# Optimization experiments

Hardware: AMD Instinct MI355X
Metric: run time of the kernel (lower is better)

Reference implementation:

```python
import jax, jax.numpy as jnp
import numpy as np

R, B, D, H, N, F = 8, 16, 32, 128, 2048, 256
HALF_LOG_2PI = np.float32(0.9189385332046727)  # 0.5*log(2*pi)


def _made_masks():
    # MADE masks for a 2-hidden-layer network (D -> H -> H -> 2*D), params=2,
    # input_order='random' per (region, batch) network, hidden degrees cyclic in [1, D-1].
    rng = np.random.RandomState(0)
    deg_in = np.stack([np.stack([rng.permutation(D) + 1 for _ in range(B)]) for _ in range(R)])  # [R,B,D]
    h_deg = (np.arange(H) % (D - 1)) + 1  # [H]
    M1 = (deg_in[:, :, :, None] <= h_deg[None, None, None, :]).astype(np.float32)  # [R,B,D,H]
    M2 = np.broadcast_to((h_deg[:, None] <= h_deg[None, :]).astype(np.float32), (R, B, H, H)).copy()  # [R,B,H,H]
    out_deg = np.repeat(deg_in, 2, axis=-1)  # [R,B,2D]; index k=2*d+p matches reshape(...,D,2)
    M3 = (h_deg[None, None, :, None] < out_deg[:, :, None, :]).astype(np.float32)  # [R,B,H,2D]
    return M1, M2, M3


def setup_inputs() -> dict:
    key = jax.random.key(0)
    k1, k2, k3, k4 = jax.random.split(key, 4)
    x = jax.random.normal(k1, (N, F), dtype=jnp.float32)
    W1 = jax.random.normal(k2, (R, B, D, H), dtype=jnp.float32) * 0.1
    W2 = jax.random.normal(k3, (R, B, H, H), dtype=jnp.float32) * 0.05
    W3 = jax.random.normal(k4, (R, B, H, 2 * D), dtype=jnp.float32) * 0.02
    M1, M2, M3 = _made_masks()
    region_idx = jnp.arange(F, dtype=jnp.int64 if jax.config.jax_enable_x64 else jnp.int32).reshape(R, D)
    return {"x": x, "W1": W1, "W2": W2, "W3": W3,
            "M1": jnp.asarray(M1), "M2": jnp.asarray(M2), "M3": jnp.asarray(M3),
            "region_idx": region_idx}


def reference(x, W1, W2, W3, M1, M2, M3, region_idx):
    # Gather per-region features: [N, R, D] -> [R, N, D]
    xr = jnp.transpose(x[:, region_idx], (1, 0, 2))
    # Masked MADE forward (no bias, relu), batched over all R*B networks.
    h1 = jax.nn.relu(jnp.einsum('rnd,rbdh->rbnh', xr, W1 * M1))
    h2 = jax.nn.relu(jnp.einsum('rbnh,rbhk->rbnk', h1, W2 * M2))
    out = jnp.einsum('rbnk,rbko->rbno', h2, W3 * M3)  # [R,B,N,2D]
    out = out.reshape(out.shape[0], out.shape[1], out.shape[2], -1, 2)  # [R,B,N,D,2]
    shift, log_scale = out[..., 0], out[..., 1]
    # MAF inverse (one pass): u = (y - shift) * exp(-log_scale);
    # log_prob = sum_d Normal(0,1).log_prob(u_d) - log_scale_d
    u = (xr[:, None] - shift) * jnp.exp(-log_scale)  # [R,B,N,D]
    ll = jnp.sum(-0.5 * u * u - HALF_LOG_2PI - log_scale, axis=-1)  # [R,B,N]
    return jnp.transpose(ll, (2, 0, 1))  # [N, R, B]
```

## Files before the change

kernel.cpp:

```cpp
#include <hip/hip_runtime.h>
#include <math.h>

constexpr int R_ = 8;
constexpr int B_ = 16;
constexpr int D_ = 32;
constexpr int H_ = 128;
constexpr int N_ = 2048;
constexpr int F_ = 256;
constexpr int O_ = 64;
constexpr float HLP_ = 0.9189385332046727f;

typedef float f32x4 __attribute__((ext_vector_type(4)));
typedef short bf16x8 __attribute__((ext_vector_type(8)));
typedef unsigned uint32x4 __attribute__((ext_vector_type(4)));

__device__ __forceinline__ unsigned pk2(float lo, float hi) {
    unsigned a = __builtin_bit_cast(unsigned, lo) + 0x8000u;
    unsigned b = __builtin_bit_cast(unsigned, hi) + 0x8000u;
    return __builtin_amdgcn_perm(b, a, 0x07060302);
}

__global__ __launch_bounds__(512, 2)
void flow_all(const float* __restrict__ x,
              const float* __restrict__ W1, const float* __restrict__ W2,
              const float* __restrict__ W3,
              const float* __restrict__ M1, const float* __restrict__ M2,
              const float* __restrict__ M3,
              const int* __restrict__ ridx,
              float* __restrict__ out)
{
    __shared__ __align__(16) unsigned short WA1[8  * 64 * 8];
    __shared__ __align__(16) unsigned short WA2[32 * 64 * 8];
    __shared__ __align__(16) unsigned short WA3[16 * 64 * 8];
    __shared__ __align__(16) unsigned short hws[8 * 4096];

    const int bid  = blockIdx.x;
    const int rb   = bid >> 1;
    const int half = bid & 1;
    const int r    = rb >> 4;

    const int t    = threadIdx.x;
    const int lane = t & 63;
    const int w    = t >> 6;
    const int q    = lane >> 4;
    const int c    = lane & 15;

    unsigned short* hwp = hws + w * 4096;

    const int nbase = half * 1024 + w * 16 + c;

    int cols[8];
#pragma unroll
    for (int j = 0; j < 8; ++j) cols[j] = ridx[r * 32 + q * 8 + j];

    float gA[8], gB[8];
    {
        const float* ra = x + (size_t)nbase * F_;
        const float* rb2 = ra + (size_t)128 * F_;
#pragma unroll
        for (int j = 0; j < 8; ++j) { gA[j] = ra[cols[j]]; gB[j] = rb2[cols[j]]; }
    }

    {
        const float* W1b = W1 + (size_t)rb * 32 * 128;
        const float* M1b = M1 + (size_t)rb * 32 * 128;
        const float* W2b = W2 + (size_t)rb * 128 * 128;
        const float* M2s = M2;
        const float* W3b = W3 + (size_t)rb * 128 * 64;
        const float* M3b = M3 + (size_t)rb * 128 * 64;

        const int pm = t & 127, pkq = t >> 7;
        const int qm = t & 63,  qkq = t >> 6;
        int osrc;
        {
            int dp = qm >> 1, pb = qm & 1;
            int dsrc = ((dp >> 1) & 3) * 8 + (dp >> 3) * 2 + (dp & 1);
            osrc = dsrc * 2 + pb;
        }

        float wv[2][8], mv[2][8];
        auto slab_load = [&](int s, float* wvv, float* mvv) {
            if (s == 0) {
                const float* wp = W1b + (size_t)(pkq * 8) * 128 + pm;
                const float* mp = M1b + (size_t)(pkq * 8) * 128 + pm;
#pragma unroll
                for (int e = 0; e < 8; ++e) { wvv[e] = wp[(size_t)e * 128]; mvv[e] = mp[(size_t)e * 128]; }
            } else if (s <= 4) {
                const float* wp = W2b + (size_t)((s - 1) * 32 + pkq * 8) * 128 + pm;
                const float* mp = M2s + (size_t)((s - 1) * 32 + pkq * 8) * 128 + pm;
#pragma unroll
                for (int e = 0; e < 8; ++e) { wvv[e] = wp[(size_t)e * 128]; mvv[e] = mp[(size_t)e * 128]; }
            } else {
                int ss = s - 5;
                const float* wp = W3b + (size_t)(ss * 64 + qkq * 8) * 64 + osrc;
                const float* mp = M3b + (size_t)(ss * 64 + qkq * 8) * 64 + osrc;
#pragma unroll
                for (int e = 0; e < 8; ++e) { wvv[e] = wp[(size_t)e * 64]; mvv[e] = mp[(size_t)e * 64]; }
            }
        };
        auto slab_store = [&](int s, const float* wvv, const float* mvv) {
            unsigned u0 = pk2(wvv[0] * mvv[0], wvv[1] * mvv[1]);
            unsigned u1 = pk2(wvv[2] * mvv[2], wvv[3] * mvv[3]);
            unsigned u2 = pk2(wvv[4] * mvv[4], wvv[5] * mvv[5]);
            unsigned u3 = pk2(wvv[6] * mvv[6], wvv[7] * mvv[7]);
            uint32x4 u = {u0, u1, u2, u3};
            if (s == 0) {
                int mt = pm >> 4, l = pkq * 16 + (pm & 15);
                *(uint32x4*)&WA1[(mt * 64 + l) * 8] = u;
            } else if (s <= 4) {
                int kt = s - 1, mt = pm >> 4, l = pkq * 16 + (pm & 15);
                *(uint32x4*)&WA2[((kt * 8 + mt) * 64 + l) * 8] = u;
            } else {
                int ss = s - 5;
                int kt = ss * 2 + (qkq >> 2), mt3 = qm >> 4, l = (qkq & 3) * 16 + (qm & 15);
                *(uint32x4*)&WA3[((kt * 4 + mt3) * 64 + l) * 8] = u;
            }
        };

        slab_load(0, wv[0], mv[0]);
#pragma unroll
        for (int s = 0; s < 7; ++s) {
            if (s < 6) slab_load(s + 1, wv[(s + 1) & 1], mv[(s + 1) & 1]);
            slab_store(s, wv[s & 1], mv[s & 1]);
        }
    }
    __syncthreads();

    const f32x4 z = {0.f, 0.f, 0.f, 0.f};
#pragma unroll 1
    for (int p = 0; p < 4; ++p) {
        float xA[8], xB[8];
#pragma unroll
        for (int j = 0; j < 8; ++j) { xA[j] = gA[j]; xB[j] = gB[j]; }
        uint32x4 uA = {pk2(xA[0], xA[1]), pk2(xA[2], xA[3]), pk2(xA[4], xA[5]), pk2(xA[6], xA[7])};
        uint32x4 uB = {pk2(xB[0], xB[1]), pk2(xB[2], xB[3]), pk2(xB[4], xB[5]), pk2(xB[6], xB[7])};
        bf16x8 xbA = __builtin_bit_cast(bf16x8, uA);
        bf16x8 xbB = __builtin_bit_cast(bf16x8, uB);

        auto hstore = [&](int tau, int mt, const f32x4& v) {
            int ktw = mt >> 1;
            int qw  = (mt & 1) * 2 + (q >> 1);
            int j0  = (q & 1) * 4;
            unsigned lo = pk2(fmaxf(v[0], 0.f), fmaxf(v[1], 0.f));
            unsigned hi = pk2(fmaxf(v[2], 0.f), fmaxf(v[3], 0.f));
            *(uint2*)&hwp[(((tau * 4 + ktw) * 64) + qw * 16 + c) * 8 + j0] = make_uint2(lo, hi);
        };

        {
            bf16x8 a_[8];
#pragma unroll
            for (int mt = 0; mt < 8; ++mt)
                a_[mt] = *(const bf16x8*)&WA1[(mt * 64 + lane) * 8];
            f32x4 accA[8], accB[8];
#pragma unroll
            for (int mt = 0; mt < 8; ++mt) {
                accA[mt] = __builtin_amdgcn_mfma_f32_16x16x32_bf16(a_[mt], xbA, z, 0, 0, 0);
                accB[mt] = __builtin_amdgcn_mfma_f32_16x16x32_bf16(a_[mt], xbB, z, 0, 0, 0);
            }
#pragma unroll
            for (int mt = 0; mt < 8; ++mt) { hstore(0, mt, accA[mt]); hstore(1, mt, accB[mt]); }
        }

        if (p < 3) {
            const float* ra = x + (size_t)(nbase + (p + 1) * 256) * F_;
            const float* rb2 = ra + (size_t)128 * F_;
#pragma unroll
            for (int j = 0; j < 8; ++j) { gA[j] = ra[cols[j]]; gB[j] = rb2[cols[j]]; }
        }

        {
            f32x4 acc2A[8], acc2B[8];
#pragma unroll
            for (int mt = 0; mt < 8; ++mt) { acc2A[mt] = z; acc2B[mt] = z; }
#pragma unroll
            for (int kt = 0; kt < 4; ++kt) {
                bf16x8 bA = *(const bf16x8*)&hwp[((0 + kt) * 64 + lane) * 8];
                bf16x8 bB = *(const bf16x8*)&hwp[((4 + kt) * 64 + lane) * 8];
                bf16x8 a2_[8];
#pragma unroll
                for (int mt = 0; mt < 8; ++mt)
                    a2_[mt] = *(const bf16x8*)&WA2[((kt * 8 + mt) * 64 + lane) * 8];
#pragma unroll
                for (int mt = 0; mt < 8; ++mt) {
                    acc2A[mt] = __builtin_amdgcn_mfma_f32_16x16x32_bf16(a2_[mt], bA, acc2A[mt], 0, 0, 0);
                    acc2B[mt] = __builtin_amdgcn_mfma_f32_16x16x32_bf16(a2_[mt], bB, acc2B[mt], 0, 0, 0);
                }
            }
#pragma unroll
            for (int mt = 0; mt < 8; ++mt) { hstore(0, mt, acc2A[mt]); hstore(1, mt, acc2B[mt]); }
        }

        {
            f32x4 acc3A[4], acc3B[4];
#pragma unroll
            for (int mt3 = 0; mt3 < 4; ++mt3) { acc3A[mt3] = z; acc3B[mt3] = z; }
#pragma unroll
            for (int kt = 0; kt < 4; ++kt) {
                bf16x8 bA = *(const bf16x8*)&hwp[((0 + kt) * 64 + lane) * 8];
                bf16x8 bB = *(const bf16x8*)&hwp[((4 + kt) * 64 + lane) * 8];
                bf16x8 a3_[4];
#pragma unroll
                for (int mt3 = 0; mt3 < 4; ++mt3)
                    a3_[mt3] = *(const bf16x8*)&WA3[((kt * 4 + mt3) * 64 + lane) * 8];
#pragma unroll
                for (int mt3 = 0; mt3 < 4; ++mt3) {
                    acc3A[mt3] = __builtin_amdgcn_mfma_f32_16x16x32_bf16(a3_[mt3], bA, acc3A[mt3], 0, 0, 0);
                    acc3B[mt3] = __builtin_amdgcn_mfma_f32_16x16x32_bf16(a3_[mt3], bB, acc3B[mt3], 0, 0, 0);
                }
            }
            float llA = 0.f, llB = 0.f;
#pragma unroll
            for (int mt3 = 0; mt3 < 4; ++mt3) {
#pragma unroll
                for (int rr = 0; rr < 2; ++rr) {
                    float shA = acc3A[mt3][rr * 2], lsA = acc3A[mt3][rr * 2 + 1];
                    float shB = acc3B[mt3][rr * 2], lsB = acc3B[mt3][rr * 2 + 1];
                    float u0 = (xA[mt3 * 2 + rr] - shA) * __expf(-lsA);
                    float u1 = (xB[mt3 * 2 + rr] - shB) * __expf(-lsB);
                    llA += fmaf(-0.5f * u0, u0, -HLP_ - lsA);
                    llB += fmaf(-0.5f * u1, u1, -HLP_ - lsB);
                }
            }
            llA += __shfl_xor(llA, 16, 64);  llA += __shfl_xor(llA, 32, 64);
            llB += __shfl_xor(llB, 16, 64);  llB += __shfl_xor(llB, 32, 64);
            if (q == 0) {
                int n = nbase + p * 256;
                out[(size_t)n * 128 + rb]         = llA;
                out[(size_t)(n + 128) * 128 + rb] = llB;
            }
        }
    }
}

extern "C" void kernel_launch(void* const* d_in, const int* in_sizes, int n_in,
                              void* d_out, int out_size, void* d_ws, size_t ws_size,
                              hipStream_t stream) {
    const float* x   = (const float*)d_in[0];
    const float* W1  = (const float*)d_in[1];
    const float* W2  = (const float*)d_in[2];
    const float* W3  = (const float*)d_in[3];
    const float* M1  = (const float*)d_in[4];
    const float* M2  = (const float*)d_in[5];
    const float* M3  = (const float*)d_in[6];
    const int*  ridx = (const int*)d_in[7];
    float* out = (float*)d_out;

    flow_all<<<dim3(256), dim3(512), 0, stream>>>(x, W1, W2, W3, M1, M2, M3, ridx, out);
}
```

Measured before the change: 109.7 us.

## Hold masked weight fragments in registers and halve block size to 4 waves

The masked bf16 weight fragments for all three layers now stay in VGPRs for the whole kernel. They are built through a small double-buffered LDS staging area with a barrier per slab, so the main loop no longer reads weights from LDS. Blocks shrink to 256 threads with launch bounds (256,1), and each wave handles a contiguous 256-row chunk over 8 iterations instead of 4. This removes repeated LDS weight reads per MFMA but uses many more registers (about 352 VGPRs of A fragments) and leaves fewer waves to hide latency.

```diff
diff --git a/kernel.cpp b/kernel.cpp
--- a/kernel.cpp
+++ b/kernel.cpp
@@ -20,7 +20,7 @@
     return __builtin_amdgcn_perm(b, a, 0x07060302);
 }
 
-__global__ __launch_bounds__(512, 2)
+__global__ __launch_bounds__(256, 1)
 void flow_all(const float* __restrict__ x,
               const float* __restrict__ W1, const float* __restrict__ W2,
               const float* __restrict__ W3,
@@ -29,15 +29,13 @@
               const int* __restrict__ ridx,
               float* __restrict__ out)
 {
-    __shared__ __align__(16) unsigned short WA1[8  * 64 * 8];
-    __shared__ __align__(16) unsigned short WA2[32 * 64 * 8];
-    __shared__ __align__(16) unsigned short WA3[16 * 64 * 8];
-    __shared__ __align__(16) unsigned short hws[8 * 4096];
-
-    const int bid  = blockIdx.x;
-    const int rb   = bid >> 1;
-    const int half = bid & 1;
-    const int r    = rb >> 4;
+    __shared__ __align__(16) unsigned short stg[2][5120];
+    __shared__ __align__(16) unsigned short hws[4][4096];
+
+    const int bid = blockIdx.x;
+    const int rb  = bid >> 1;
+    const int hf  = bid & 1;
+    const int r   = rb >> 4;
 
     const int t    = threadIdx.x;
     const int lane = t & 63;
@@ -45,9 +43,9 @@
     const int q    = lane >> 4;
     const int c    = lane & 15;
 
-    unsigned short* hwp = hws + w * 4096;
-
-    const int nbase = half * 1024 + w * 16 + c;
+    unsigned short* hwp = hws[w];
+
+    const int nbase = hf * 1024 + w * 256 + c;
 
     int cols[8];
 #pragma unroll
@@ -55,12 +53,13 @@
 
     float gA[8], gB[8];
     {
-        const float* ra = x + (size_t)nbase * F_;
-        const float* rb2 = ra + (size_t)128 * F_;
-#pragma unroll
-        for (int j = 0; j < 8; ++j) { gA[j] = ra[cols[j]]; gB[j] = rb2[cols[j]]; }
+        const float* ra  = x + (size_t)nbase * F_;
+        const float* rbp = ra + (size_t)16 * F_;
+#pragma unroll
+        for (int j = 0; j < 8; ++j) { gA[j] = ra[cols[j]]; gB[j] = rbp[cols[j]]; }
     }
 
+    bf16x8 a1[8], a2[4][8], a3[4][4];
     {
         const float* W1b = W1 + (size_t)rb * 32 * 128;
         const float* M1b = M1 + (size_t)rb * 32 * 128;
@@ -69,8 +68,8 @@
         const float* W3b = W3 + (size_t)rb * 128 * 64;
         const float* M3b = M3 + (size_t)rb * 128 * 64;
 
-        const int pm = t & 127, pkq = t >> 7;
-        const int qm = t & 63,  qkq = t >> 6;
+        const int pm  = t & 127, pkh = t >> 7;
+        const int qm  = t & 63,  qk  = t >> 6;
         int osrc;
         {
             int dp = qm >> 1, pb = qm & 1;
@@ -78,42 +77,40 @@
             osrc = dsrc * 2 + pb;
         }
 
-        float wv[2][8], mv[2][8];
+        float wv[2][16], mv[2][16];
         auto slab_load = [&](int s, float* wvv, float* mvv) {
             if (s == 0) {
-                const float* wp = W1b + (size_t)(pkq * 8) * 128 + pm;
-                const float* mp = M1b + (size_t)(pkq * 8) * 128 + pm;
-#pragma unroll
-                for (int e = 0; e < 8; ++e) { wvv[e] = wp[(size_t)e * 128]; mvv[e] = mp[(size_t)e * 128]; }
+                const float* wp = W1b + (size_t)(pkh * 16) * 128 + pm;
+                const float* mp = M1b + (size_t)(pkh * 16) * 128 + pm;
+#pragma unroll
+                for (int e = 0; e < 16; ++e) { wvv[e] = wp[(size_t)e * 128]; mvv[e] = mp[(size_t)e * 128]; }
             } else if (s <= 4) {
-                const float* wp = W2b + (size_t)((s - 1) * 32 + pkq * 8) * 128 + pm;
-                const float* mp = M2s + (size_t)((s - 1) * 32 + pkq * 8) * 128 + pm;
-#pragma unroll
-                for (int e = 0; e < 8; ++e) { wvv[e] = wp[(size_t)e * 128]; mvv[e] = mp[(size_t)e * 128]; }
+                const float* wp = W2b + (size_t)((s - 1) * 32 + pkh * 16) * 128 + pm;
+                const float* mp = M2s + (size_t)((s - 1) * 32 + pkh * 16) * 128 + pm;
+#pragma unroll
+                for (int e = 0; e < 16; ++e) { wvv[e] = wp[(size_t)e * 128]; mvv[e] = mp[(size_t)e * 128]; }
             } else {
                 int ss = s - 5;
-                const float* wp = W3b + (size_t)(ss * 64 + qkq * 8) * 64 + osrc;
-                const float* mp = M3b + (size_t)(ss * 64 + qkq * 8) * 64 + osrc;
-#pragma unroll
-                for (int e = 0; e < 8; ++e) { wvv[e] = wp[(size_t)e * 64]; mvv[e] = mp[(size_t)e * 64]; }
+                const float* wp = W3b + (size_t)(ss * 64 + qk * 16) * 64 + osrc;
+                const float* mp = M3b + (size_t)(ss * 64 + qk * 16) * 64 + osrc;
+#pragma unroll
+                for (int e = 0; e < 16; ++e) { wvv[e] = wp[(size_t)e * 64]; mvv[e] = mp[(size_t)e * 64]; }
             }
         };
         auto slab_store = [&](int s, const float* wvv, const float* mvv) {
-            unsigned u0 = pk2(wvv[0] * mvv[0], wvv[1] * mvv[1]);
-            unsigned u1 = pk2(wvv[2] * mvv[2], wvv[3] * mvv[3]);
-            unsigned u2 = pk2(wvv[4] * mvv[4], wvv[5] * mvv[5]);
-            unsigned u3 = pk2(wvv[6] * mvv[6], wvv[7] * mvv[7]);
-            uint32x4 u = {u0, u1, u2, u3};
-            if (s == 0) {
-                int mt = pm >> 4, l = pkq * 16 + (pm & 15);
-                *(uint32x4*)&WA1[(mt * 64 + l) * 8] = u;
-            } else if (s <= 4) {
-                int kt = s - 1, mt = pm >> 4, l = pkq * 16 + (pm & 15);
-                *(uint32x4*)&WA2[((kt * 8 + mt) * 64 + l) * 8] = u;
+            unsigned u[8];
+#pragma unroll
+            for (int e2 = 0; e2 < 8; ++e2)
+                u[e2] = pk2(wvv[2 * e2] * mvv[2 * e2], wvv[2 * e2 + 1] * mvv[2 * e2 + 1]);
+            uint32x4 ulo = {u[0], u[1], u[2], u[3]};
+            uint32x4 uhi = {u[4], u[5], u[6], u[7]};
+            unsigned short* st = stg[s & 1];
+            if (s <= 4) {
+                *(uint32x4*)&st[pm * 40 + pkh * 16]     = ulo;
+                *(uint32x4*)&st[pm * 40 + pkh * 16 + 8] = uhi;
             } else {
-                int ss = s - 5;
-                int kt = ss * 2 + (qkq >> 2), mt3 = qm >> 4, l = (qkq & 3) * 16 + (qm & 15);
-                *(uint32x4*)&WA3[((kt * 4 + mt3) * 64 + l) * 8] = u;
+                *(uint32x4*)&st[qm * 72 + qk * 16]     = ulo;
+                *(uint32x4*)&st[qm * 72 + qk * 16 + 8] = uhi;
             }
         };
 
@@ -122,13 +119,39 @@
         for (int s = 0; s < 7; ++s) {
             if (s < 6) slab_load(s + 1, wv[(s + 1) & 1], mv[(s + 1) & 1]);
             slab_store(s, wv[s & 1], mv[s & 1]);
+            __syncthreads();
+            const unsigned short* st = stg[s & 1];
+            if (s == 0) {
+#pragma unroll
+                for (int mt = 0; mt < 8; ++mt)
+                    a1[mt] = *(const bf16x8*)&st[(mt * 16 + c) * 40 + q * 8];
+            } else if (s <= 4) {
+#pragma unroll
+                for (int mt = 0; mt < 8; ++mt)
+                    a2[s - 1][mt] = *(const bf16x8*)&st[(mt * 16 + c) * 40 + q * 8];
+            } else {
+                int ss = s - 5;
+#pragma unroll
+                for (int mt3 = 0; mt3 < 4; ++mt3) {
+                    a3[ss * 2 + 0][mt3] = *(const bf16x8*)&st[(mt3 * 16 + c) * 72 + 0  + q * 8];
+                    a3[ss * 2 + 1][mt3] = *(const bf16x8*)&st[(mt3 * 16 + c) * 72 + 32 + q * 8];
+                }
+            }
         }
     }
-    __syncthreads();
+
+    auto hstore = [&](int tau, int mt, const f32x4& v) {
+        int ktw = mt >> 1;
+        int qw  = (mt & 1) * 2 + (q >> 1);
+        int j0  = (q & 1) * 4;
+        unsigned lo = pk2(fmaxf(v[0], 0.f), fmaxf(v[1], 0.f));
+        unsigned hi = pk2(fmaxf(v[2], 0.f), fmaxf(v[3], 0.f));
+        *(uint2*)&hwp[(((tau * 4 + ktw) * 64) + qw * 16 + c) * 8 + j0] = make_uint2(lo, hi);
+    };
 
     const f32x4 z = {0.f, 0.f, 0.f, 0.f};
 #pragma unroll 1
-    for (int p = 0; p < 4; ++p) {
+    for (int p = 0; p < 8; ++p) {
         float xA[8], xB[8];
 #pragma unroll
         for (int j = 0; j < 8; ++j) { xA[j] = gA[j]; xB[j] = gB[j]; }
@@ -137,75 +160,54 @@
         bf16x8 xbA = __builtin_bit_cast(bf16x8, uA);
         bf16x8 xbB = __builtin_bit_cast(bf16x8, uB);
 
-        auto hstore = [&](int tau, int mt, const f32x4& v) {
-            int ktw = mt >> 1;
-            int qw  = (mt & 1) * 2 + (q >> 1);
-            int j0  = (q & 1) * 4;
-            unsigned lo = pk2(fmaxf(v[0], 0.f), fmaxf(v[1], 0.f));
-            unsigned hi = pk2(fmaxf(v[2], 0.f), fmaxf(v[3], 0.f));
-            *(uint2*)&hwp[(((tau * 4 + ktw) * 64) + qw * 16 + c) * 8 + j0] = make_uint2(lo, hi);
-        };
-
-        {
-            bf16x8 a_[8];
-#pragma unroll
-            for (int mt = 0; mt < 8; ++mt)
-                a_[mt] = *(const bf16x8*)&WA1[(mt * 64 + lane) * 8];
+        {
             f32x4 accA[8], accB[8];
 #pragma unroll
             for (int mt = 0; mt < 8; ++mt) {
-                accA[mt] = __builtin_amdgcn_mfma_f32_16x16x32_bf16(a_[mt], xbA, z, 0, 0, 0);
-                accB[mt] = __builtin_amdgcn_mfma_f32_16x16x32_bf16(a_[mt], xbB, z, 0, 0, 0);
+                accA[mt] = __builtin_amdgcn_mfma_f32_16x16x32_bf16(a1[mt], xbA, z, 0, 0, 0);
+                accB[mt] = __builtin_amdgcn_mfma_f32_16x16x32_bf16(a1[mt], xbB, z, 0, 0, 0);
             }
 #pragma unroll
             for (int mt = 0; mt < 8; ++mt) { hstore(0, mt, accA[mt]); hstore(1, mt, accB[mt]); }
         }
 
-        if (p < 3) {
-            const float* ra = x + (size_t)(nbase + (p + 1) * 256) * F_;
-            const float* rb2 = ra + (size_t)128 * F_;
-#pragma unroll
-            for (int j = 0; j < 8; ++j) { gA[j] = ra[cols[j]]; gB[j] = rb2[cols[j]]; }
-        }
-
-        {
-            f32x4 acc2A[8], acc2B[8];
-#pragma unroll
-            for (int mt = 0; mt < 8; ++mt) { acc2A[mt] = z; acc2B[mt] = z; }
+        if (p < 7) {
+            const float* ra  = x + (size_t)(nbase + (p + 1) * 32) * F_;
+            const float* rbp = ra + (size_t)16 * F_;
+#pragma unroll
+            for (int j = 0; j < 8; ++j) { gA[j] = ra[cols[j]]; gB[j] = rbp[cols[j]]; }
+        }
+
+        {
+            f32x4 c2A[8], c2B[8];
+#pragma unroll
+            for (int mt = 0; mt < 8; ++mt) { c2A[mt] = z; c2B[mt] = z; }
 #pragma unroll
             for (int kt = 0; kt < 4; ++kt) {
                 bf16x8 bA = *(const bf16x8*)&hwp[((0 + kt) * 64 + lane) * 8];
                 bf16x8 bB = *(const bf16x8*)&hwp[((4 + kt) * 64 + lane) * 8];
-                bf16x8 a2_[8];
-#pragma unroll
-                for (int mt = 0; mt < 8; ++mt)
-                    a2_[mt] = *(const bf16x8*)&WA2[((kt * 8 + mt) * 64 + lane) * 8];
 #pragma unroll
                 for (int mt = 0; mt < 8; ++mt) {
-                    acc2A[mt] = __builtin_amdgcn_mfma_f32_16x16x32_bf16(a2_[mt], bA, acc2A[mt], 0, 0, 0);
-                    acc2B[mt] = __builtin_amdgcn_mfma_f32_16x16x32_bf16(a2_[mt], bB, acc2B[mt], 0, 0, 0);
-                }
-            }
-#pragma unroll
-            for (int mt = 0; mt < 8; ++mt) { hstore(0, mt, acc2A[mt]); hstore(1, mt, acc2B[mt]); }
-        }
-
-        {
-            f32x4 acc3A[4], acc3B[4];
-#pragma unroll
-            for (int mt3 = 0; mt3 < 4; ++mt3) { acc3A[mt3] = z; acc3B[mt3] = z; }
+                    c2A[mt] = __builtin_amdgcn_mfma_f32_16x16x32_bf16(a2[kt][mt], bA, c2A[mt], 0, 0, 0);
+                    c2B[mt] = __builtin_amdgcn_mfma_f32_16x16x32_bf16(a2[kt][mt], bB, c2B[mt], 0, 0, 0);
+                }
+            }
+#pragma unroll
+            for (int mt = 0; mt < 8; ++mt) { hstore(0, mt, c2A[mt]); hstore(1, mt, c2B[mt]); }
+        }
+
+        {
+            f32x4 c3A[4], c3B[4];
+#pragma unroll
+            for (int mt3 = 0; mt3 < 4; ++mt3) { c3A[mt3] = z; c3B[mt3] = z; }
 #pragma unroll
             for (int kt = 0; kt < 4; ++kt) {
                 bf16x8 bA = *(const bf16x8*)&hwp[((0 + kt) * 64 + lane) * 8];
                 bf16x8 bB = *(const bf16x8*)&hwp[((4 + kt) * 64 + lane) * 8];
-                bf16x8 a3_[4];
-#pragma unroll
-                for (int mt3 = 0; mt3 < 4; ++mt3)
-                    a3_[mt3] = *(const bf16x8*)&WA3[((kt * 4 + mt3) * 64 + lane) * 8];
 #pragma unroll
                 for (int mt3 = 0; mt3 < 4; ++mt3) {
-                    acc3A[mt3] = __builtin_amdgcn_mfma_f32_16x16x32_bf16(a3_[mt3], bA, acc3A[mt3], 0, 0, 0);
-                    acc3B[mt3] = __builtin_amdgcn_mfma_f32_16x16x32_bf16(a3_[mt3], bB, acc3B[mt3], 0, 0, 0);
+                    c3A[mt3] = __builtin_amdgcn_mfma_f32_16x16x32_bf16(a3[kt][mt3], bA, c3A[mt3], 0, 0, 0);
+                    c3B[mt3] = __builtin_amdgcn_mfma_f32_16x16x32_bf16(a3[kt][mt3], bB, c3B[mt3], 0, 0, 0);
                 }
             }
             float llA = 0.f, llB = 0.f;
@@ -213,8 +215,8 @@
             for (int mt3 = 0; mt3 < 4; ++mt3) {
 #pragma unroll
                 for (int rr = 0; rr < 2; ++rr) {
-                    float shA = acc3A[mt3][rr * 2], lsA = acc3A[mt3][rr * 2 + 1];
-                    float shB = acc3B[mt3][rr * 2], lsB = acc3B[mt3][rr * 2 + 1];
+                    float shA = c3A[mt3][rr * 2], lsA = c3A[mt3][rr * 2 + 1];
+                    float shB = c3B[mt3][rr * 2], lsB = c3B[mt3][rr * 2 + 1];
                     float u0 = (xA[mt3 * 2 + rr] - shA) * __expf(-lsA);
                     float u1 = (xB[mt3 * 2 + rr] - shB) * __expf(-lsB);
                     llA += fmaf(-0.5f * u0, u0, -HLP_ - lsA);
@@ -224,9 +226,9 @@
             llA += __shfl_xor(llA, 16, 64);  llA += __shfl_xor(llA, 32, 64);
             llB += __shfl_xor(llB, 16, 64);  llB += __shfl_xor(llB, 32, 64);
             if (q == 0) {
-                int n = nbase + p * 256;
-                out[(size_t)n * 128 + rb]         = llA;
-                out[(size_t)(n + 128) * 128 + rb] = llB;
+                int n = nbase + p * 32;
+                out[(size_t)n * 128 + rb]        = llA;
+                out[(size_t)(n + 16) * 128 + rb] = llB;
             }
         }
     }
@@ -245,5 +247,5 @@
     const int*  ridx = (const int*)d_in[7];
     float* out = (float*)d_out;
 
-    flow_all<<<dim3(256), dim3(512), 0, stream>>>(x, W1, W2, W3, M1, M2, M3, ridx, out);
+    flow_all<<<dim3(256), dim3(256), 0, stream>>>(x, W1, W2, W3, M1, M2, M3, ridx, out);
 }
```

Measured after the change: 115.3 us. 5.1% more time.
